# Performance work log

Measured on AMD Instinct MI355X. Metric: run time of the kernel, lower is better.

Reference implementation:

```python
import jax, jax.numpy as jnp
import numpy as np

DIM = 1024
NUM_HEADS = 16
HEAD_DIM = DIM // NUM_HEADS
SCALE = HEAD_DIM ** -0.5


def setup_inputs() -> dict:
    key = jax.random.key(0)
    k_x, k_qkv, k_pw, k_pb = jax.random.split(key, 4)
    B, N, C = 1, 4096, 3 * DIM
    x = jax.random.normal(k_x, (B, N, C), dtype=jnp.float32)
    # torch nn.Linear stores weight as [out, in]; y = x @ W.T + b
    W_qkv = jax.random.normal(k_qkv, (3 * DIM, 3 * DIM), dtype=jnp.float32) * (3 * DIM) ** -0.5
    W_proj = jax.random.normal(k_pw, (DIM, DIM), dtype=jnp.float32) * DIM ** -0.5
    b_proj = jax.random.normal(k_pb, (DIM,), dtype=jnp.float32) * 0.01
    return {"x": x, "W_qkv": W_qkv, "W_proj": W_proj, "b_proj": b_proj}


def reference(x, W_qkv, W_proj, b_proj):
    B, N, C = x.shape  # C == 3*DIM
    qkv = x @ W_qkv.T  # [B, N, 3*DIM]
    qkv = qkv.reshape(B, N, 3, NUM_HEADS, HEAD_DIM).transpose(2, 0, 3, 1, 4)
    q, k, v = qkv[0], qkv[1], qkv[2]  # each [B, H, N, hd]
    attn = jnp.einsum('bhnd,bhmd->bhnm', q, k) * SCALE
    attn = jax.nn.softmax(attn, axis=-1)
    out = jnp.einsum('bhnm,bhmd->bhnd', attn, v)  # [B, H, N, hd]
    out = out.transpose(0, 2, 1, 3).reshape(B, N, DIM)
    return out @ W_proj.T + b_proj
```

## Files before the change

### kernel.cpp

```cpp
#include <hip/hip_runtime.h>
#include <hip/hip_fp16.h>

#define SEQ     4096
#define NHEADS  16
#define HDIM    64
#define DIMSZ   1024
#define ATT_SCALE 0.125f

static constexpr size_t QSZ = (size_t)NHEADS * SEQ * HDIM;

typedef __attribute__((ext_vector_type(8))) short short8;
typedef __attribute__((ext_vector_type(4))) short s16x4;
typedef __attribute__((ext_vector_type(8))) unsigned short ushort8;
typedef __attribute__((ext_vector_type(4))) float f32x4;
#define MFMA_F16(a, b, c) __builtin_amdgcn_mfma_f32_16x16x32_f16((a), (b), (c), 0, 0, 0)

__device__ __forceinline__ unsigned short f2hu(float x) {
    __half h = __float2half(x);
    return *reinterpret_cast<unsigned short*>(&h);
}
__device__ __forceinline__ float hu2f(unsigned short u) {
    __half h = *reinterpret_cast<__half*>(&u);
    return __half2float(h);
}
__device__ __forceinline__ void split8h(float4 f0, float4 f1, ushort8& h, ushort8& l) {
    const float v[8] = {f0.x, f0.y, f0.z, f0.w, f1.x, f1.y, f1.z, f1.w};
    #pragma unroll
    for (int i = 0; i < 8; ++i) {
        const unsigned short hi = f2hu(v[i]);
        h[i] = hi;
        l[i] = f2hu(v[i] - hu2f(hi));
    }
}

typedef __attribute__((address_space(1))) const unsigned int g_u32;
typedef __attribute__((address_space(3))) unsigned int lds_u32;
__device__ __forceinline__ void async16(unsigned short* lds, const unsigned short* g) {
    __builtin_amdgcn_global_load_lds((g_u32*)g, (lds_u32*)lds, 16, 0, 0);
}

__global__ void prep_split(const float* __restrict__ x, unsigned short* __restrict__ xh,
                           unsigned short* __restrict__ xl, int nx,
                           const float* __restrict__ w0, unsigned short* __restrict__ w0h,
                           int n0,
                           const float* __restrict__ w1, unsigned short* __restrict__ w1h,
                           int n1)
{
    const int stride = gridDim.x * blockDim.x;
    const int tid = blockIdx.x * blockDim.x + threadIdx.x;
    for (int i = tid; i < (nx >> 2); i += stride) {
        float4 v = ((const float4*)x)[i];
        ushort4 h, l;
        h.x = f2hu(v.x); l.x = f2hu(v.x - hu2f(h.x));
        h.y = f2hu(v.y); l.y = f2hu(v.y - hu2f(h.y));
        h.z = f2hu(v.z); l.z = f2hu(v.z - hu2f(h.z));
        h.w = f2hu(v.w); l.w = f2hu(v.w - hu2f(h.w));
        ((ushort4*)xh)[i] = h; ((ushort4*)xl)[i] = l;
    }
    for (int i = tid; i < (n0 >> 2); i += stride) {
        float4 v = ((const float4*)w0)[i];
        ushort4 h;
        h.x = f2hu(v.x); h.y = f2hu(v.y); h.z = f2hu(v.z); h.w = f2hu(v.w);
        ((ushort4*)w0h)[i] = h;
    }
    for (int i = tid; i < (n1 >> 2); i += stride) {
        float4 v = ((const float4*)w1)[i];
        ushort4 h;
        h.x = f2hu(v.x); h.y = f2hu(v.y); h.z = f2hu(v.z); h.w = f2hu(v.w);
        ((ushort4*)w1h)[i] = h;
    }
}

__global__ __launch_bounds__(512, 2)
void qkv_gemm_8ph(const unsigned short* __restrict__ AHg,
                  const unsigned short* __restrict__ ALg,
                  const unsigned short* __restrict__ BHg,
                  unsigned short* __restrict__ QH, unsigned short* __restrict__ QL,
                  unsigned short* __restrict__ KH, unsigned short* __restrict__ VT)
{
    constexpr int K3 = 3072;
    constexpr int NT = K3 / 32;
    __shared__ __align__(16) unsigned short ring[3 * 24576];

    const int t  = threadIdx.x;
    const int wv = t >> 6;
    const int ln = t & 63;
    const int lx = ln & 15;
    const int q4 = ln >> 4;
    const int wr = wv >> 2;
    const int wc = wv & 3;

    const int bid = blockIdx.x;
    const int swz = (bid & 7) * 32 + (bid >> 3);
    const int m0 = (swz >> 4) * 256;
    const int n0 = (swz & 15) * 192;

    const int srow = t >> 2;
    const int sg8  = (((t & 3) ^ ((t >> 3) & 3)) << 3);

    auto stage3a = [&](int tt, int b) {
        const int kk = tt << 5;
        unsigned short* Lb = &ring[b * 24576 + wv * 512];
        const size_t ga = (size_t)(m0 + srow) * K3 + kk + sg8;
        async16(Lb,               AHg + ga);
        async16(Lb + 4096,        AHg + ga + (size_t)128 * K3);
        async16(Lb + 8192,        ALg + ga);
    };
    auto stage3b = [&](int tt, int b) {
        const int kk = tt << 5;
        unsigned short* Lb = &ring[b * 24576 + wv * 512];
        const size_t ga = (size_t)(m0 + srow) * K3 + kk + sg8;
        const size_t gb = (size_t)(n0 + srow) * K3 + kk + sg8;
        async16(Lb + 12288,       ALg + ga + (size_t)128 * K3);
        async16(Lb + 16384,       BHg + gb);
        async16(Lb + 20480,       BHg + gb + (size_t)128 * K3);
    };

    f32x4 acc[8][3];
    #pragma unroll
    for (int mf = 0; mf < 8; ++mf)
        #pragma unroll
        for (int nf = 0; nf < 3; ++nf)
            acc[mf][nf] = (f32x4){0.f, 0.f, 0.f, 0.f};

    stage3a(0, 0); stage3b(0, 0);
    stage3a(1, 1); stage3b(1, 1);
    asm volatile("s_waitcnt vmcnt(6)" ::: "memory");
    __builtin_amdgcn_s_barrier();

    const int aswz8 = ((q4 ^ ((lx >> 1) & 3)) << 3);
    const int arow0 = (wr * 128 + lx) * 32 + aswz8;
    const int brow0 = (wc * 48  + lx) * 32 + aswz8;

    int c = 0;
    for (int kt = 0; kt < NT; ++kt) {
        const unsigned short* AHp = &ring[c * 24576];
        const unsigned short* ALp = AHp + 8192;
        const unsigned short* Bp  = AHp + 16384;
        int c2 = c + 2; if (c2 >= 3) c2 -= 3;
        const bool pf = (kt + 2 < NT);

        short8 bfr[3];
        #pragma unroll
        for (int ph = 0; ph < 4; ++ph) {
            if (ph == 0) {
                #pragma unroll
                for (int nf = 0; nf < 3; ++nf)
                    bfr[nf] = *(const short8*)&Bp[brow0 + nf * 512];
            }
            short8 ahf[2], alf[2];
            #pragma unroll
            for (int i = 0; i < 2; ++i) {
                const int mo = arow0 + (ph * 2 + i) * 512;
                ahf[i] = *(const short8*)&AHp[mo];
                alf[i] = *(const short8*)&ALp[mo];
            }
            if (ph == 0 && pf) stage3a(kt + 2, c2);
            if (ph == 1 && pf) stage3b(kt + 2, c2);
            __builtin_amdgcn_s_setprio(1);
            #pragma unroll
            for (int nf = 0; nf < 3; ++nf)
                #pragma unroll
                for (int i = 0; i < 2; ++i) {
                    acc[ph * 2 + i][nf] = MFMA_F16(ahf[i], bfr[nf], acc[ph * 2 + i][nf]);
                    acc[ph * 2 + i][nf] = MFMA_F16(alf[i], bfr[nf], acc[ph * 2 + i][nf]);
                }
            __builtin_amdgcn_s_setprio(0);
            if (ph == 3) {
                if (pf) asm volatile("s_waitcnt vmcnt(6)" ::: "memory");
                else    asm volatile("s_waitcnt vmcnt(0)" ::: "memory");
                __builtin_amdgcn_s_barrier();
            }
        }
        ++c; if (c == 3) c = 0;
    }

    #pragma unroll
    for (int nf = 0; nf < 3; ++nf) {
        const int colb = n0 + wc * 48 + nf * 16;
        const int part = colb >> 10;
        const int head = (colb >> 6) & 15;
        const int d0   = (colb & 63) + lx;
        if (part == 0) {
            #pragma unroll
            for (int mf = 0; mf < 8; ++mf) {
                const int row0 = m0 + wr * 128 + mf * 16 + q4 * 4;
                #pragma unroll
                for (int r = 0; r < 4; ++r) {
                    const float v = acc[mf][nf][r] * ATT_SCALE;
                    const unsigned short h = f2hu(v);
                    const size_t idx = ((size_t)head * SEQ + row0 + r) * HDIM + d0;
                    QH[idx] = h;
                    QL[idx] = f2hu(v - hu2f(h));
                }
            }
        } else if (part == 1) {
            #pragma unroll
            for (int mf = 0; mf < 8; ++mf) {
                const int row0 = m0 + wr * 128 + mf * 16 + q4 * 4;
                #pragma unroll
                for (int r = 0; r < 4; ++r) {
                    const size_t idx = ((size_t)head * SEQ + row0 + r) * HDIM + d0;
                    KH[idx] = f2hu(acc[mf][nf][r]);
                }
            }
        } else {
            unsigned short* base = VT + ((size_t)head * HDIM + d0) * SEQ;
            #pragma unroll
            for (int mf = 0; mf < 8; ++mf) {
                const int row0 = m0 + wr * 128 + mf * 16 + q4 * 4;
                ushort4 o;
                o.x = f2hu(acc[mf][nf][0]); o.y = f2hu(acc[mf][nf][1]);
                o.z = f2hu(acc[mf][nf][2]); o.w = f2hu(acc[mf][nf][3]);
                *(ushort4*)(base + row0) = o;
            }
        }
    }
}

template <int MODE, bool ASPLIT>
__global__ __launch_bounds__(256, 3)
void mfma_gemm_abt(const float* __restrict__ A,
                   const unsigned short* __restrict__ AHg,
                   const unsigned short* __restrict__ ALg,
                   const unsigned short* __restrict__ BHg,
                   const float* __restrict__ bias, float* __restrict__ C,
                   unsigned short* __restrict__ QH, unsigned short* __restrict__ QL,
                   unsigned short* __restrict__ KH, unsigned short* __restrict__ VT,
                   int M, int N, int K)
{
    constexpr int LDP = ASPLIT ? 32 : 40;
    __shared__ unsigned short AHs[128 * LDP];
    __shared__ unsigned short ALs[128 * LDP];
    __shared__ unsigned short BHs[128 * LDP];

    const int t  = threadIdx.x;
    const int wv = t >> 6;
    const int ln = t & 63;
    const int lx = ln & 15;
    const int q4 = ln >> 4;
    const int m0 = blockIdx.y * 128;
    const int n0 = blockIdx.x * 128;

    f32x4 acc[2][8];
    #pragma unroll
    for (int mf = 0; mf < 2; ++mf)
        #pragma unroll
        for (int nf = 0; nf < 8; ++nf)
            acc[mf][nf] = (f32x4){0.f, 0.f, 0.f, 0.f};

    for (int k0 = 0; k0 < K; k0 += 32) {
        if constexpr (ASPLIT) {
            const int rowc = ln >> 2;
            const int c8   = (ln & 3) << 3;
            #pragma unroll
            for (int rep = 0; rep < 2; ++rep) {
                const int chunk = rep * 4 + wv;
                const int r = chunk * 16 + rowc;
                const size_t goff = (size_t)(m0 + r) * K + k0 + c8;
                const size_t boff = (size_t)(n0 + r) * K + k0 + c8;
                async16(&AHs[chunk * 16 * LDP], AHg + goff);
                async16(&ALs[chunk * 16 * LDP], ALg + goff);
                async16(&BHs[chunk * 16 * LDP], BHg + boff);
            }
        } else {
            #pragma unroll
            for (int rep = 0; rep < 2; ++rep) {
                const int task = rep * 256 + t;
                const int r  = task >> 2;
                const int sg = (task & 3) << 3;
                {
                    const float* p = A + (size_t)(m0 + r) * K + k0 + sg;
                    float4 f0 = *(const float4*)p;
                    float4 f1 = *(const float4*)(p + 4);
                    ushort8 h, l; split8h(f0, f1, h, l);
                    *(ushort8*)&AHs[r * LDP + sg] = h;
                    *(ushort8*)&ALs[r * LDP + sg] = l;
                }
                {
                    const size_t off = (size_t)(n0 + r) * K + k0 + sg;
                    *(ushort8*)&BHs[r * LDP + sg] = *(const ushort8*)(BHg + off);
                }
            }
        }
        __syncthreads();

        short8 ah[2], al[2];
        #pragma unroll
        for (int mf = 0; mf < 2; ++mf) {
            const int row = wv * 32 + mf * 16 + lx;
            ah[mf] = *(const short8*)&AHs[row * LDP + q4 * 8];
            al[mf] = *(const short8*)&ALs[row * LDP + q4 * 8];
        }
        #pragma unroll
        for (int nf = 0; nf < 8; ++nf) {
            const short8 bh = *(const short8*)&BHs[(nf * 16 + lx) * LDP + q4 * 8];
            #pragma unroll
            for (int mf = 0; mf < 2; ++mf) {
                acc[mf][nf] = MFMA_F16(ah[mf], bh, acc[mf][nf]);
                acc[mf][nf] = MFMA_F16(al[mf], bh, acc[mf][nf]);
            }
        }
        __syncthreads();
    }

    if constexpr (MODE == 0) {
        #pragma unroll
        for (int nf = 0; nf < 8; ++nf) {
            const int col = n0 + nf * 16 + lx;
            const float bv = bias[col];
            #pragma unroll
            for (int mf = 0; mf < 2; ++mf) {
                const int row0 = m0 + wv * 32 + mf * 16 + q4 * 4;
                #pragma unroll
                for (int r = 0; r < 4; ++r)
                    C[(size_t)(row0 + r) * N + col] = acc[mf][nf][r] + bv;
            }
        }
    } else {
        const int part = n0 >> 10;
        #pragma unroll
        for (int nf = 0; nf < 8; ++nf) {
            const int colb = n0 + nf * 16;
            const int head = (colb >> 6) & 15;
            const int d0   = (colb & 63) + lx;
            if (part == 0) {
                #pragma unroll
                for (int mf = 0; mf < 2; ++mf) {
                    const int row0 = m0 + wv * 32 + mf * 16 + q4 * 4;
                    #pragma unroll
                    for (int r = 0; r < 4; ++r) {
                        const float v = acc[mf][nf][r] * ATT_SCALE;
                        const unsigned short h = f2hu(v);
                        const size_t idx = ((size_t)head * SEQ + row0 + r) * HDIM + d0;
                        QH[idx] = h;
                        QL[idx] = f2hu(v - hu2f(h));
                    }
                }
            } else if (part == 1) {
                #pragma unroll
                for (int mf = 0; mf < 2; ++mf) {
                    const int row0 = m0 + wv * 32 + mf * 16 + q4 * 4;
                    #pragma unroll
                    for (int r = 0; r < 4; ++r) {
                        const size_t idx = ((size_t)head * SEQ + row0 + r) * HDIM + d0;
                        KH[idx] = f2hu(acc[mf][nf][r]);
                    }
                }
            } else {
                unsigned short* base = VT + ((size_t)head * HDIM + d0) * SEQ;
                #pragma unroll
                for (int mf = 0; mf < 2; ++mf) {
                    const int row0 = m0 + wv * 32 + mf * 16 + q4 * 4;
                    ushort4 o;
                    o.x = f2hu(acc[mf][nf][0]); o.y = f2hu(acc[mf][nf][1]);
                    o.z = f2hu(acc[mf][nf][2]); o.w = f2hu(acc[mf][nf][3]);
                    *(ushort4*)(base + row0) = o;
                }
            }
        }
    }
}

__global__ __launch_bounds__(256, 2)
void attn_mfma(const unsigned short* __restrict__ QHg,
               const unsigned short* __restrict__ QLg,
               const unsigned short* __restrict__ KHg,
               const unsigned short* __restrict__ VTg,
               unsigned short* __restrict__ AttnH,
               unsigned short* __restrict__ AttnL)
{
    __shared__ __align__(16) char shraw[65536];
    unsigned short* KA = (unsigned short*)shraw;
    unsigned short* VA = (unsigned short*)(shraw + 16384);
    unsigned short* KB = (unsigned short*)(shraw + 32768);
    unsigned short* VB = (unsigned short*)(shraw + 49152);
    float* obuf = (float*)shraw;
    float* lbuf = (float*)(shraw + 34816);

    const int t  = threadIdx.x;
    const int wv = t >> 6;
    const int ln = t & 63;
    const int q4 = ln >> 4;
    const int lx = ln & 15;
    const int qb   = blockIdx.x;
    const int head = blockIdx.y;

    const unsigned short* Kh = KHg + (size_t)head * SEQ * HDIM;
    const unsigned short* Vg = VTg + (size_t)head * HDIM * SEQ;

    short8 qh[4][2], ql[4][2];
    #pragma unroll
    for (int qt = 0; qt < 4; ++qt)
        #pragma unroll
        for (int s = 0; s < 2; ++s) {
            const size_t off = ((size_t)head * SEQ + (size_t)qb * 64 + qt * 16 + lx) * HDIM
                             + s * 32 + q4 * 8;
            qh[qt][s] = *(const short8*)(QHg + off);
            ql[qt][s] = *(const short8*)(QLg + off);
        }

    f32x4 o_acc[4][4];
    float l_part[4] = {0.f, 0.f, 0.f, 0.f};
    #pragma unroll
    for (int dt = 0; dt < 4; ++dt)
        #pragma unroll
        for (int qt = 0; qt < 4; ++qt)
            o_acc[dt][qt] = (f32x4){0.f, 0.f, 0.f, 0.f};

    const int rK8 = t >> 3;
    const int gck = ((t & 7) ^ (rK8 & 7)) << 3;
    const int rV4 = t >> 4;
    const int gcv = ((t & 15) ^ (rV4 & 7)) << 3;

    auto issue_tile = [&](int kbase, unsigned short* KX, unsigned short* VX) {
        #pragma unroll
        for (int c = 0; c < 4; ++c) {
            async16(KX + (c * 32 + wv * 8) * 64,
                    Kh + (size_t)(kbase + c * 32 + rK8) * HDIM + gck);
            async16(VX + (c * 16 + wv * 4) * 128,
                    Vg + (size_t)(c * 16 + rV4) * SEQ + kbase + gcv);
        }
    };

    auto compute_tile = [&](const unsigned short* KX, const unsigned short* VX) {
        short8 phi[4];
        #pragma unroll
        for (int st = 0; st < 2; ++st) {
            const int kr = st * 64 + wv * 16 + lx;
            short8 kfh[2];
            #pragma unroll
            for (int s = 0; s < 2; ++s)
                kfh[s] = *(const short8*)&KX[kr * 64 + (((s * 4 + q4) ^ (kr & 7)) << 3)];
            #pragma unroll
            for (int qt = 0; qt < 4; ++qt) {
                f32x4 sa = (f32x4){0.f, 0.f, 0.f, 0.f};
                __builtin_amdgcn_s_setprio(1);
                #pragma unroll
                for (int s = 0; s < 2; ++s) {
                    sa = MFMA_F16(kfh[s], qh[qt][s], sa);
                    sa = MFMA_F16(kfh[s], ql[qt][s], sa);
                }
                __builtin_amdgcn_s_setprio(0);
                #pragma unroll
                for (int r = 0; r < 4; ++r) {
                    const float e = __expf(sa[r]);
                    l_part[qt] += e;
                    phi[qt][st * 4 + r] = (short)f2hu(e);
                }
            }
        }
        const int colb = wv * 32 + q4 * 8;
        const int sl0  = colb >> 4;
        const int sub  = (colb & 15) >> 1;
        #pragma unroll
        for (int dt = 0; dt < 4; ++dt) {
            const int vr = dt * 16 + lx;
            const s16x4 v0 = *(const s16x4*)&VX[vr * 128 + (((sl0    ) ^ (vr & 7)) << 3) + sub];
            const s16x4 v1 = *(const s16x4*)&VX[vr * 128 + (((sl0 + 8) ^ (vr & 7)) << 3) + sub];
            short8 vf;
            #pragma unroll
            for (int i = 0; i < 4; ++i) { vf[i] = v0[i]; vf[i + 4] = v1[i]; }
            __builtin_amdgcn_s_setprio(1);
            #pragma unroll
            for (int qt = 0; qt < 4; ++qt)
                o_acc[dt][qt] = MFMA_F16(vf, phi[qt], o_acc[dt][qt]);
            __builtin_amdgcn_s_setprio(0);
        }
    };

    issue_tile(0, KA, VA);
    __syncthreads();

    for (int i = 0; i < SEQ / 256; ++i) {
        const int mt = 2 * i;
        if (mt + 1 < SEQ / 128) issue_tile((mt + 1) * 128, KB, VB);
        compute_tile(KA, VA);
        __syncthreads();
        if (mt + 2 < SEQ / 128) issue_tile((mt + 2) * 128, KA, VA);
        compute_tile(KB, VB);
        __syncthreads();
    }

    float lw[4];
    #pragma unroll
    for (int qt = 0; qt < 4; ++qt) {
        float l = l_part[qt];
        l += __shfl_xor(l, 16);
        l += __shfl_xor(l, 32);
        lw[qt] = l;
    }
    if (q4 == 0) {
        #pragma unroll
        for (int qt = 0; qt < 4; ++qt)
            lbuf[wv * 64 + qt * 16 + lx] = lw[qt];
    }
    #pragma unroll
    for (int p = 0; p < 2; ++p) {
        #pragma unroll
        for (int dd = 0; dd < 2; ++dd) {
            const int dt = p * 2 + dd;
            #pragma unroll
            for (int qt = 0; qt < 4; ++qt)
                #pragma unroll
                for (int r = 0; r < 4; ++r)
                    obuf[wv * 2176 + (dd * 16 + q4 * 4 + r) * 68 + qt * 16 + lx]
                        = o_acc[dt][qt][r];
        }
        __syncthreads();
        {
            const int q  = t >> 2;
            const int dg = (t & 3) << 3;
            const float linv = 1.f / (lbuf[q] + lbuf[64 + q] + lbuf[128 + q] + lbuf[192 + q]);
            ushort8 ho, lo;
            #pragma unroll
            for (int j = 0; j < 8; ++j) {
                const int dloc = dg + j;
                const float s = obuf[dloc * 68 + q] + obuf[2176 + dloc * 68 + q]
                              + obuf[4352 + dloc * 68 + q] + obuf[6528 + dloc * 68 + q];
                const float v = s * linv;
                const unsigned short h = f2hu(v);
                ho[j] = (short)h;
                lo[j] = (short)f2hu(v - hu2f(h));
            }
            const size_t ob = (size_t)(qb * 64 + q) * DIMSZ + head * HDIM + p * 32 + dg;
            *(ushort8*)(AttnH + ob) = ho;
            *(ushort8*)(AttnL + ob) = lo;
        }
        __syncthreads();
    }
}

extern "C" void kernel_launch(void* const* d_in, const int* in_sizes, int n_in,
                              void* d_out, int out_size, void* d_ws,
                              size_t ws_size, hipStream_t stream)
{
    const float* x     = (const float*)d_in[0];
    const float* Wqkv  = (const float*)d_in[1];
    const float* Wproj = (const float*)d_in[2];
    const float* bproj = (const float*)d_in[3];
    float* out = (float*)d_out;

    const size_t NWQ = (size_t)3072 * 3072;
    const size_t NWP = (size_t)1024 * 1024;
    const size_t NX  = (size_t)4096 * 3072;

    unsigned short* ub = (unsigned short*)d_ws;
    unsigned short* AttnH = ub;
    unsigned short* AttnL = ub + QSZ;
    unsigned short* QHg = ub + 2 * QSZ;
    unsigned short* QLg = ub + 3 * QSZ;
    unsigned short* KHg = ub + 4 * QSZ;
    unsigned short* VTg = ub + 5 * QSZ;
    unsigned short* WQH = ub + 6 * QSZ;
    unsigned short* WPH = WQH + NWQ;
    unsigned short* XH  = WPH + NWP;
    unsigned short* XL  = XH + NX;
    const bool xsplit = ws_size >= 121634816ull;

    prep_split<<<2048, 256, 0, stream>>>(
        xsplit ? x : nullptr, XH, XL, xsplit ? (int)NX : 0,
        Wqkv, WQH, (int)NWQ, Wproj, WPH, (int)NWP);

    if (xsplit) {
        qkv_gemm_8ph<<<256, 512, 0, stream>>>(
            XH, XL, WQH, QHg, QLg, KHg, VTg);
    } else {
        dim3 g1(3 * DIMSZ / 128, SEQ / 128);
        mfma_gemm_abt<1, false><<<g1, 256, 0, stream>>>(
            x, nullptr, nullptr, WQH, nullptr, nullptr,
            QHg, QLg, KHg, VTg, SEQ, 3 * DIMSZ, 3 * DIMSZ);
    }

    dim3 g2(SEQ / 64, NHEADS);
    attn_mfma<<<g2, 256, 0, stream>>>(QHg, QLg, KHg, VTg, AttnH, AttnL);

    dim3 g3(DIMSZ / 128, SEQ / 128);
    mfma_gemm_abt<0, true><<<g3, 256, 0, stream>>>(
        nullptr, AttnH, AttnL, WPH, bproj, out,
        nullptr, nullptr, nullptr, nullptr, SEQ, DIMSZ, DIMSZ);
}
```

Measured before the change: 404.1 us.

## Switch QKV GEMM to 32x32x16 MFMA with 4x2 wave tiling

```diff
diff --git a/kernel.cpp b/kernel.cpp
--- a/kernel.cpp
+++ b/kernel.cpp
@@ -13,7 +13,9 @@
 typedef __attribute__((ext_vector_type(4))) short s16x4;
 typedef __attribute__((ext_vector_type(8))) unsigned short ushort8;
 typedef __attribute__((ext_vector_type(4))) float f32x4;
+typedef __attribute__((ext_vector_type(16))) float f32x16;
 #define MFMA_F16(a, b, c) __builtin_amdgcn_mfma_f32_16x16x32_f16((a), (b), (c), 0, 0, 0)
+#define MFMA32_F16(a, b, c) __builtin_amdgcn_mfma_f32_32x32x16_f16((a), (b), (c), 0, 0, 0)
 
 __device__ __forceinline__ unsigned short f2hu(float x) {
     __half h = __float2half(x);
@@ -85,10 +87,10 @@
     const int t  = threadIdx.x;
     const int wv = t >> 6;
     const int ln = t & 63;
-    const int lx = ln & 15;
-    const int q4 = ln >> 4;
-    const int wr = wv >> 2;
-    const int wc = wv & 3;
+    const int l31 = ln & 31;
+    const int hi  = ln >> 5;
+    const int wr = wv >> 1;
+    const int wc = wv & 1;
 
     const int bid = blockIdx.x;
     const int swz = (bid & 7) * 32 + (bid >> 3);
@@ -116,21 +118,28 @@
         async16(Lb + 20480,       BHg + gb + (size_t)128 * K3);
     };
 
-    f32x4 acc[8][3];
-    #pragma unroll
-    for (int mf = 0; mf < 8; ++mf)
+    f32x16 acc[2][3];
+    #pragma unroll
+    for (int mf = 0; mf < 2; ++mf)
         #pragma unroll
         for (int nf = 0; nf < 3; ++nf)
-            acc[mf][nf] = (f32x4){0.f, 0.f, 0.f, 0.f};
+            #pragma unroll
+            for (int e = 0; e < 16; ++e)
+                acc[mf][nf][e] = 0.f;
 
     stage3a(0, 0); stage3b(0, 0);
     stage3a(1, 1); stage3b(1, 1);
     asm volatile("s_waitcnt vmcnt(6)" ::: "memory");
     __builtin_amdgcn_s_barrier();
 
-    const int aswz8 = ((q4 ^ ((lx >> 1) & 3)) << 3);
-    const int arow0 = (wr * 128 + lx) * 32 + aswz8;
-    const int brow0 = (wc * 48  + lx) * 32 + aswz8;
+    const int wsz = (l31 >> 1) & 3;
+    const int so0 = ((0 * 2 + hi) ^ wsz) * 8;
+    const int so1 = ((1 * 2 + hi) ^ wsz) * 8;
+    int arow[2], brow[3];
+    #pragma unroll
+    for (int mf = 0; mf < 2; ++mf) arow[mf] = (wr * 64 + mf * 32 + l31) * 32;
+    #pragma unroll
+    for (int nf = 0; nf < 3; ++nf) brow[nf] = (wc * 96 + nf * 32 + l31) * 32;
 
     int c = 0;
     for (int kt = 0; kt < NT; ++kt) {
@@ -140,79 +149,80 @@
         int c2 = c + 2; if (c2 >= 3) c2 -= 3;
         const bool pf = (kt + 2 < NT);
 
-        short8 bfr[3];
-        #pragma unroll
-        for (int ph = 0; ph < 4; ++ph) {
-            if (ph == 0) {
-                #pragma unroll
-                for (int nf = 0; nf < 3; ++nf)
-                    bfr[nf] = *(const short8*)&Bp[brow0 + nf * 512];
-            }
-            short8 ahf[2], alf[2];
-            #pragma unroll
-            for (int i = 0; i < 2; ++i) {
-                const int mo = arow0 + (ph * 2 + i) * 512;
-                ahf[i] = *(const short8*)&AHp[mo];
-                alf[i] = *(const short8*)&ALp[mo];
-            }
-            if (ph == 0 && pf) stage3a(kt + 2, c2);
-            if (ph == 1 && pf) stage3b(kt + 2, c2);
-            __builtin_amdgcn_s_setprio(1);
-            #pragma unroll
-            for (int nf = 0; nf < 3; ++nf)
-                #pragma unroll
-                for (int i = 0; i < 2; ++i) {
-                    acc[ph * 2 + i][nf] = MFMA_F16(ahf[i], bfr[nf], acc[ph * 2 + i][nf]);
-                    acc[ph * 2 + i][nf] = MFMA_F16(alf[i], bfr[nf], acc[ph * 2 + i][nf]);
-                }
-            __builtin_amdgcn_s_setprio(0);
-            if (ph == 3) {
-                if (pf) asm volatile("s_waitcnt vmcnt(6)" ::: "memory");
-                else    asm volatile("s_waitcnt vmcnt(0)" ::: "memory");
-                __builtin_amdgcn_s_barrier();
-            }
-        }
+        if (pf) stage3a(kt + 2, c2);
+        short8 bh[3][2];
+        #pragma unroll
+        for (int nf = 0; nf < 3; ++nf) {
+            bh[nf][0] = *(const short8*)&Bp[brow[nf] + so0];
+            bh[nf][1] = *(const short8*)&Bp[brow[nf] + so1];
+        }
+        if (pf) stage3b(kt + 2, c2);
+        short8 ahf[2][2], alf[2][2];
+        #pragma unroll
+        for (int mf = 0; mf < 2; ++mf) {
+            ahf[mf][0] = *(const short8*)&AHp[arow[mf] + so0];
+            ahf[mf][1] = *(const short8*)&AHp[arow[mf] + so1];
+            alf[mf][0] = *(const short8*)&ALp[arow[mf] + so0];
+            alf[mf][1] = *(const short8*)&ALp[arow[mf] + so1];
+        }
+        __builtin_amdgcn_s_setprio(1);
+        #pragma unroll
+        for (int nf = 0; nf < 3; ++nf)
+            #pragma unroll
+            for (int mf = 0; mf < 2; ++mf)
+                #pragma unroll
+                for (int s = 0; s < 2; ++s) {
+                    acc[mf][nf] = MFMA32_F16(ahf[mf][s], bh[nf][s], acc[mf][nf]);
+                    acc[mf][nf] = MFMA32_F16(alf[mf][s], bh[nf][s], acc[mf][nf]);
+                }
+        __builtin_amdgcn_s_setprio(0);
+        if (pf) asm volatile("s_waitcnt vmcnt(6)" ::: "memory");
+        else    asm volatile("s_waitcnt vmcnt(0)" ::: "memory");
+        __builtin_amdgcn_s_barrier();
         ++c; if (c == 3) c = 0;
     }
 
     #pragma unroll
     for (int nf = 0; nf < 3; ++nf) {
-        const int colb = n0 + wc * 48 + nf * 16;
+        const int colb = n0 + wc * 96 + nf * 32;
         const int part = colb >> 10;
         const int head = (colb >> 6) & 15;
-        const int d0   = (colb & 63) + lx;
-        if (part == 0) {
-            #pragma unroll
-            for (int mf = 0; mf < 8; ++mf) {
-                const int row0 = m0 + wr * 128 + mf * 16 + q4 * 4;
-                #pragma unroll
-                for (int r = 0; r < 4; ++r) {
-                    const float v = acc[mf][nf][r] * ATT_SCALE;
-                    const unsigned short h = f2hu(v);
-                    const size_t idx = ((size_t)head * SEQ + row0 + r) * HDIM + d0;
-                    QH[idx] = h;
-                    QL[idx] = f2hu(v - hu2f(h));
-                }
-            }
-        } else if (part == 1) {
-            #pragma unroll
-            for (int mf = 0; mf < 8; ++mf) {
-                const int row0 = m0 + wr * 128 + mf * 16 + q4 * 4;
-                #pragma unroll
-                for (int r = 0; r < 4; ++r) {
-                    const size_t idx = ((size_t)head * SEQ + row0 + r) * HDIM + d0;
-                    KH[idx] = f2hu(acc[mf][nf][r]);
-                }
-            }
-        } else {
-            unsigned short* base = VT + ((size_t)head * HDIM + d0) * SEQ;
-            #pragma unroll
-            for (int mf = 0; mf < 8; ++mf) {
-                const int row0 = m0 + wr * 128 + mf * 16 + q4 * 4;
-                ushort4 o;
-                o.x = f2hu(acc[mf][nf][0]); o.y = f2hu(acc[mf][nf][1]);
-                o.z = f2hu(acc[mf][nf][2]); o.w = f2hu(acc[mf][nf][3]);
-                *(ushort4*)(base + row0) = o;
+        const int d0   = (colb & 63) + l31;
+        #pragma unroll
+        for (int mf = 0; mf < 2; ++mf) {
+            const int rbase = m0 + wr * 64 + mf * 32 + 4 * hi;
+            if (part == 0) {
+                #pragma unroll
+                for (int g = 0; g < 4; ++g)
+                    #pragma unroll
+                    for (int j = 0; j < 4; ++j) {
+                        const int row = rbase + 8 * g + j;
+                        const float v = acc[mf][nf][4 * g + j] * ATT_SCALE;
+                        const unsigned short h = f2hu(v);
+                        const size_t idx = ((size_t)head * SEQ + row) * HDIM + d0;
+                        QH[idx] = h;
+                        QL[idx] = f2hu(v - hu2f(h));
+                    }
+            } else if (part == 1) {
+                #pragma unroll
+                for (int g = 0; g < 4; ++g)
+                    #pragma unroll
+                    for (int j = 0; j < 4; ++j) {
+                        const int row = rbase + 8 * g + j;
+                        const size_t idx = ((size_t)head * SEQ + row) * HDIM + d0;
+                        KH[idx] = f2hu(acc[mf][nf][4 * g + j]);
+                    }
+            } else {
+                unsigned short* base = VT + ((size_t)head * HDIM + d0) * SEQ;
+                #pragma unroll
+                for (int g = 0; g < 4; ++g) {
+                    ushort4 o;
+                    o.x = f2hu(acc[mf][nf][4 * g]);
+                    o.y = f2hu(acc[mf][nf][4 * g + 1]);
+                    o.z = f2hu(acc[mf][nf][4 * g + 2]);
+                    o.w = f2hu(acc[mf][nf][4 * g + 3]);
+                    *(ushort4*)(base + rbase + 8 * g) = o;
+                }
             }
         }
     }
```

Result: slower. 432.9 us (+7.1%).
